# Kernel tuning notes

Hardware: AMD Instinct MI355X
Metric: run time of the kernel (lower is better)

Reference implementation:

```python
import jax, jax.numpy as jnp
import numpy as np

B, T, C, A, P = 16, 1024, 512, 4096, 256  # batch, frames, phones, allophone arcs, phonemes


def setup_inputs() -> dict:
    key = jax.random.key(0)
    k1, k2, k3 = jax.random.split(key, 3)
    hs_pad = jax.random.normal(k1, (B, T, C), dtype=jnp.float32)
    # each phone has exactly A // C allophone arcs (full coverage, balanced)
    phone_arc_labels = jnp.arange(A, dtype=jnp.int32) % C
    arcs_per_phone = A // C
    # weights near -log(arcs_per_phone) so sum_a exp(log_prob + w) ~= 1,
    # matching a trained allophone layer and keeping the redis step log-safe
    alloW = 0.01 * jax.random.normal(k2, (A,), dtype=jnp.float32) - jnp.log(
        jnp.float32(arcs_per_phone)
    )
    phoneme_arc_labels = jax.random.randint(k3, (A,), 0, P, dtype=jnp.int32)
    return {
        "hs_pad": hs_pad,
        "alloW": alloW,
        "phone_arc_labels": phone_arc_labels,
        "phoneme_arc_labels": phoneme_arc_labels,
        "n_phonemes": P,
    }


def reference(hs_pad, alloW, phone_arc_labels, phoneme_arc_labels, n_phonemes):
    # log_softmax over phones
    log_probs = jax.nn.log_softmax(hs_pad, axis=-1)  # [B,T,C]
    # WFST intersection of linear emission graph with 1-state allophone graph:
    # arc a gets weight log_probs[..., phone_label(a)] + alloW[a]
    new_emissions = log_probs[..., phone_arc_labels] + alloW  # [B,T,A]
    # squash many phones per phoneme: exp + scatter-add over output labels
    ex = jnp.exp(new_emissions)
    Bq, Tq = ex.shape[0], ex.shape[1]
    squashed = jnp.zeros((Bq, Tq, n_phonemes), dtype=ex.dtype)
    squashed = squashed.at[..., phoneme_arc_labels].add(ex)  # [B,T,P]
    # redistribute probability mass so it sums to 1
    redistributed = (squashed.sum(axis=-1) - 1.0)[..., None] / n_phonemes
    squashed = squashed - redistributed
    return jnp.log(squashed)
```

## Files before the change

kernel.cpp:

```cpp
#include <hip/hip_runtime.h>
#include <hip/hip_bf16.h>

#define BT   16384
#define CDIM 512
#define ADIM 4096
#define PDIM 256

typedef __attribute__((ext_vector_type(8))) short  short8;
typedef __attribute__((ext_vector_type(8))) unsigned short ushort8;
typedef __attribute__((ext_vector_type(4))) float  f32x4;

__device__ __forceinline__ unsigned short bf16_rne(float f) {
    unsigned int u = __float_as_uint(f);
    u += 0x7FFFu + ((u >> 16) & 1u);
    return (unsigned short)(u >> 16);
}

__global__ __launch_bounds__(256) void build_Wf(const float* __restrict__ alloW,
                                                const int* __restrict__ phone_lab,
                                                const int* __restrict__ phoneme_lab,
                                                unsigned short* __restrict__ Wf) {
    __shared__ float wrow[32 * PDIM];
    const int bx = blockIdx.x;
    const int t  = threadIdx.x;

#pragma unroll
    for (int i = 0; i < 32; ++i) wrow[i * 256 + t] = 0.0f;
    __syncthreads();

#pragma unroll
    for (int i = 0; i < ADIM / 256; ++i) {
        int a = i * 256 + t;
        int c = phone_lab[a];
        if ((c >> 5) == bx)
            atomicAdd(&wrow[(c & 31) * 256 + phoneme_lab[a]], __expf(alloW[a]));
    }
    __syncthreads();

    ushort8 pk[4];
#pragma unroll
    for (int g = 0; g < 4; ++g) {
#pragma unroll
        for (int j = 0; j < 8; ++j)
            pk[g][j] = bf16_rne(wrow[(g * 8 + j) * 256 + t]);
    }
    unsigned short* dst = Wf + (size_t)bx * (PDIM * 32) + t * 32;
#pragma unroll
    for (int g = 0; g < 4; ++g)
        *(ushort8*)(dst + g * 8) = pk[g];
}

__global__ __launch_bounds__(256, 2) void allo_fused(const float* __restrict__ hs,
                                                     const unsigned short* __restrict__ Wf,
                                                     float* __restrict__ out) {
    __shared__ __align__(16) unsigned short Af[2 * 16 * 16 * 32];
    __shared__ float invZ[32];
    __shared__ float psum[4][32];

    const int tid  = threadIdx.x;
    const int wave = tid >> 6;
    const int lane = tid & 63;
    const int row0 = blockIdx.x * 32;

    {
        const int r   = tid >> 3;
        const int ksl = tid & 7;
        const int rb  = r >> 4;
        const int cc  = r & 15;
        const float* hsr = hs + (size_t)(row0 + r) * CDIM + ksl * 4;
        unsigned short* af = Af + rb * 8192 + cc * 32 + ksl * 4;

        float s = 0.0f;
#pragma unroll
        for (int h = 0; h < 2; ++h) {
            float4 v[8];
#pragma unroll
            for (int i = 0; i < 8; ++i)
                v[i] = *(const float4*)(hsr + (h * 8 + i) * 32);
#pragma unroll
            for (int i = 0; i < 8; ++i) {
                float e0 = __expf(v[i].x), e1 = __expf(v[i].y);
                float e2 = __expf(v[i].z), e3 = __expf(v[i].w);
                s += (e0 + e1) + (e2 + e3);
                ushort4 pk;
                pk.x = bf16_rne(e0); pk.y = bf16_rne(e1);
                pk.z = bf16_rne(e2); pk.w = bf16_rne(e3);
                *(ushort4*)(af + (h * 8 + i) * 512) = pk;
            }
        }
        s += __shfl_xor(s, 1);
        s += __shfl_xor(s, 2);
        s += __shfl_xor(s, 4);
        if (ksl == 0) invZ[r] = 1.0f / s;
    }
    __syncthreads();

    const int c = lane & 15;
    const int q = lane >> 4;

    f32x4 acc[2][4];
#pragma unroll
    for (int rb = 0; rb < 2; ++rb)
#pragma unroll
        for (int cb = 0; cb < 4; ++cb)
            acc[rb][cb] = (f32x4){0.f, 0.f, 0.f, 0.f};

    const unsigned short* wb  = Wf + (size_t)(wave * 64 + c) * 32 + q * 8;
    const unsigned short* af0 = Af + c * 32 + q * 8;

    short8 Bb[2][2][4];
    short8 Ab[2][2][2];

#pragma unroll
    for (int it = 0; it < 2; ++it) {
        const unsigned short* wkb = wb + it * 8192;
#pragma unroll
        for (int cb = 0; cb < 4; ++cb)
            Bb[0][it][cb] = *(const short8*)(wkb + cb * 512);
#pragma unroll
        for (int rb = 0; rb < 2; ++rb)
            Ab[0][it][rb] = *(const short8*)(af0 + rb * 8192 + it * 512);
    }

#pragma unroll
    for (int g = 0; g < 8; ++g) {
        const int cur = g & 1, nxt = cur ^ 1;
        if (g < 7) {
            const int kb0 = (g + 1) * 2;
#pragma unroll
            for (int it = 0; it < 2; ++it) {
                const unsigned short* wkb = wb + (size_t)(kb0 + it) * 8192;
#pragma unroll
                for (int cb = 0; cb < 4; ++cb)
                    Bb[nxt][it][cb] = *(const short8*)(wkb + cb * 512);
#pragma unroll
                for (int rb = 0; rb < 2; ++rb)
                    Ab[nxt][it][rb] = *(const short8*)(af0 + rb * 8192 + (kb0 + it) * 512);
            }
        }
#pragma unroll
        for (int it = 0; it < 2; ++it)
#pragma unroll
            for (int rb = 0; rb < 2; ++rb)
#pragma unroll
                for (int cb = 0; cb < 4; ++cb)
                    acc[rb][cb] = __builtin_amdgcn_mfma_f32_16x16x32_bf16(
                        Ab[cur][it][rb], Bb[cur][it][cb], acc[rb][cb], 0, 0, 0);
    }

    float sv[2][4];
#pragma unroll
    for (int rb = 0; rb < 2; ++rb)
#pragma unroll
        for (int r = 0; r < 4; ++r) {
            float x = (acc[rb][0][r] + acc[rb][1][r]) + (acc[rb][2][r] + acc[rb][3][r]);
            x += __shfl_xor(x, 1);
            x += __shfl_xor(x, 2);
            x += __shfl_xor(x, 4);
            x += __shfl_xor(x, 8);
            sv[rb][r] = x;
        }
    if (c == 0) {
#pragma unroll
        for (int rb = 0; rb < 2; ++rb)
#pragma unroll
            for (int r = 0; r < 4; ++r)
                psum[wave][rb * 16 + q * 4 + r] = sv[rb][r];
    }
    __syncthreads();

#pragma unroll
    for (int rb = 0; rb < 2; ++rb)
#pragma unroll
        for (int r = 0; r < 4; ++r) {
            const int rr = rb * 16 + q * 4 + r;
            const float iz = invZ[rr];
            const float S  = ((psum[0][rr] + psum[1][rr]) + (psum[2][rr] + psum[3][rr])) * iz;
            const float corr = (S - 1.0f) * (1.0f / (float)PDIM);
            float* orow = out + (size_t)(row0 + rr) * PDIM + wave * 64 + c;
#pragma unroll
            for (int cb = 0; cb < 4; ++cb)
                orow[cb * 16] = __logf(acc[rb][cb][r] * iz - corr);
        }
}

extern "C" void kernel_launch(void* const* d_in, const int* in_sizes, int n_in,
                              void* d_out, int out_size, void* d_ws, size_t ws_size,
                              hipStream_t stream) {
    const float* hs          = (const float*)d_in[0];
    const float* alloW       = (const float*)d_in[1];
    const int*   phone_lab   = (const int*)d_in[2];
    const int*   phoneme_lab = (const int*)d_in[3];
    float*       out         = (float*)d_out;

    unsigned short* Wf = (unsigned short*)d_ws;

    build_Wf<<<CDIM / 32, 256, 0, stream>>>(alloW, phone_lab, phoneme_lab, Wf);
    allo_fused<<<BT / 32, 256, 0, stream>>>(hs, Wf, out);
}
```

Baseline: 100.2 us.

## Process 64 rows per block with 8 waves and drop manual register prefetch

Doubles each block's tile from 32 to 64 rows and from 4 to 8 waves. The two halves of the waves cover different row halves and share the same Wf column groups, so the block count is halved. The explicit double-buffered register prefetch of the MFMA operands is replaced by a simple unroll-4 loop that leaves scheduling to the compiler. The goal is better reuse and lower per-block overhead, at the cost of fewer blocks (256 for 256 CUs) and possibly less hidden global-load latency for Wf.

```diff
diff --git a/kernel.cpp b/kernel.cpp
--- a/kernel.cpp
+++ b/kernel.cpp
@@ -50,25 +50,25 @@
         *(ushort8*)(dst + g * 8) = pk[g];
 }
 
-__global__ __launch_bounds__(256, 2) void allo_fused(const float* __restrict__ hs,
+__global__ __launch_bounds__(512, 2) void allo_fused(const float* __restrict__ hs,
                                                      const unsigned short* __restrict__ Wf,
                                                      float* __restrict__ out) {
-    __shared__ __align__(16) unsigned short Af[2 * 16 * 16 * 32];
-    __shared__ float invZ[32];
-    __shared__ float psum[4][32];
+    __shared__ __align__(16) unsigned short Af[4 * 16 * 16 * 32];
+    __shared__ float invZ[64];
+    __shared__ float psum[4][64];
 
     const int tid  = threadIdx.x;
     const int wave = tid >> 6;
     const int lane = tid & 63;
-    const int row0 = blockIdx.x * 32;
+    const int row0 = blockIdx.x * 64;
 
     {
-        const int r   = tid >> 3;
-        const int ksl = tid & 7;
-        const int rb  = r >> 4;
-        const int cc  = r & 15;
+        const int r    = tid >> 3;
+        const int ksl  = tid & 7;
+        const int rblk = r >> 4;
+        const int cc   = r & 15;
         const float* hsr = hs + (size_t)(row0 + r) * CDIM + ksl * 4;
-        unsigned short* af = Af + rb * 8192 + cc * 32 + ksl * 4;
+        unsigned short* af = Af + rblk * 8192 + cc * 32 + ksl * 4;
 
         float s = 0.0f;
 #pragma unroll
@@ -95,8 +95,10 @@
     }
     __syncthreads();
 
-    const int c = lane & 15;
-    const int q = lane >> 4;
+    const int c        = lane & 15;
+    const int q        = lane >> 4;
+    const int rowhalf  = wave >> 2;
+    const int cg       = wave & 3;
 
     f32x4 acc[2][4];
 #pragma unroll
@@ -105,47 +107,28 @@
         for (int cb = 0; cb < 4; ++cb)
             acc[rb][cb] = (f32x4){0.f, 0.f, 0.f, 0.f};
 
-    const unsigned short* wb  = Wf + (size_t)(wave * 64 + c) * 32 + q * 8;
-    const unsigned short* af0 = Af + c * 32 + q * 8;
+    const unsigned short* wb  = Wf + (size_t)(cg * 64 + c) * 32 + q * 8;
+    const unsigned short* af0 = Af + (size_t)rowhalf * 16384 + c * 32 + q * 8;
 
-    short8 Bb[2][2][4];
-    short8 Ab[2][2][2];
+#pragma unroll 4
+    for (int kb = 0; kb < 16; ++kb) {
+        short8 a0 = *(const short8*)(af0 + kb * 512);
+        short8 a1 = *(const short8*)(af0 + 8192 + kb * 512);
 
-#pragma unroll
-    for (int it = 0; it < 2; ++it) {
-        const unsigned short* wkb = wb + it * 8192;
-#pragma unroll
-        for (int cb = 0; cb < 4; ++cb)
-            Bb[0][it][cb] = *(const short8*)(wkb + cb * 512);
-#pragma unroll
-        for (int rb = 0; rb < 2; ++rb)
-            Ab[0][it][rb] = *(const short8*)(af0 + rb * 8192 + it * 512);
-    }
+        const unsigned short* wkb = wb + (size_t)kb * 8192;
+        short8 b0 = *(const short8*)(wkb);
+        short8 b1 = *(const short8*)(wkb + 512);
+        short8 b2 = *(const short8*)(wkb + 1024);
+        short8 b3 = *(const short8*)(wkb + 1536);
 
-#pragma unroll
-    for (int g = 0; g < 8; ++g) {
-        const int cur = g & 1, nxt = cur ^ 1;
-        if (g < 7) {
-            const int kb0 = (g + 1) * 2;
-#pragma unroll
-            for (int it = 0; it < 2; ++it) {
-                const unsigned short* wkb = wb + (size_t)(kb0 + it) * 8192;
-#pragma unroll
-                for (int cb = 0; cb < 4; ++cb)
-                    Bb[nxt][it][cb] = *(const short8*)(wkb + cb * 512);
-#pragma unroll
-                for (int rb = 0; rb < 2; ++rb)
-                    Ab[nxt][it][rb] = *(const short8*)(af0 + rb * 8192 + (kb0 + it) * 512);
-            }
-        }
-#pragma unroll
-        for (int it = 0; it < 2; ++it)
-#pragma unroll
-            for (int rb = 0; rb < 2; ++rb)
-#pragma unroll
-                for (int cb = 0; cb < 4; ++cb)
-                    acc[rb][cb] = __builtin_amdgcn_mfma_f32_16x16x32_bf16(
-                        Ab[cur][it][rb], Bb[cur][it][cb], acc[rb][cb], 0, 0, 0);
+        acc[0][0] = __builtin_amdgcn_mfma_f32_16x16x32_bf16(a0, b0, acc[0][0], 0, 0, 0);
+        acc[0][1] = __builtin_amdgcn_mfma_f32_16x16x32_bf16(a0, b1, acc[0][1], 0, 0, 0);
+        acc[0][2] = __builtin_amdgcn_mfma_f32_16x16x32_bf16(a0, b2, acc[0][2], 0, 0, 0);
+        acc[0][3] = __builtin_amdgcn_mfma_f32_16x16x32_bf16(a0, b3, acc[0][3], 0, 0, 0);
+        acc[1][0] = __builtin_amdgcn_mfma_f32_16x16x32_bf16(a1, b0, acc[1][0], 0, 0, 0);
+        acc[1][1] = __builtin_amdgcn_mfma_f32_16x16x32_bf16(a1, b1, acc[1][1], 0, 0, 0);
+        acc[1][2] = __builtin_amdgcn_mfma_f32_16x16x32_bf16(a1, b2, acc[1][2], 0, 0, 0);
+        acc[1][3] = __builtin_amdgcn_mfma_f32_16x16x32_bf16(a1, b3, acc[1][3], 0, 0, 0);
     }
 
     float sv[2][4];
@@ -165,7 +148,7 @@
         for (int rb = 0; rb < 2; ++rb)
 #pragma unroll
             for (int r = 0; r < 4; ++r)
-                psum[wave][rb * 16 + q * 4 + r] = sv[rb][r];
+                psum[cg][rowhalf * 32 + rb * 16 + q * 4 + r] = sv[rb][r];
     }
     __syncthreads();
 
@@ -173,11 +156,11 @@
     for (int rb = 0; rb < 2; ++rb)
 #pragma unroll
         for (int r = 0; r < 4; ++r) {
-            const int rr = rb * 16 + q * 4 + r;
+            const int rr = rowhalf * 32 + rb * 16 + q * 4 + r;
             const float iz = invZ[rr];
             const float S  = ((psum[0][rr] + psum[1][rr]) + (psum[2][rr] + psum[3][rr])) * iz;
             const float corr = (S - 1.0f) * (1.0f / (float)PDIM);
-            float* orow = out + (size_t)(row0 + rr) * PDIM + wave * 64 + c;
+            float* orow = out + (size_t)(row0 + rr) * PDIM + cg * 64 + c;
 #pragma unroll
             for (int cb = 0; cb < 4; ++cb)
                 orow[cb * 16] = __logf(acc[rb][cb][r] * iz - corr);
@@ -196,5 +179,5 @@
     unsigned short* Wf = (unsigned short*)d_ws;
 
     build_Wf<<<CDIM / 32, 256, 0, stream>>>(alloW, phone_lab, phoneme_lab, Wf);
-    allo_fused<<<BT / 32, 256, 0, stream>>>(hs, Wf, out);
+    allo_fused<<<BT / 64, 512, 0, stream>>>(hs, Wf, out);
 }
```

Result: no change. 100.1 us (-0.0%).
